# Performance work log

Hardware: AMD Instinct MI355X
Metric: run time of the kernel (lower is better)

Reference implementation:

```python
import jax, jax.numpy as jnp
import numpy as np

B, H, S, D = 2, 16, 2048, 64

def setup_inputs() -> dict:
    key = jax.random.key(0)
    kq, kk, kv = jax.random.split(key, 3)
    q = jax.random.normal(kq, (B, H, S, D), dtype=jnp.float32)
    k = jax.random.normal(kk, (B, H, S, D), dtype=jnp.float32)
    v = jax.random.normal(kv, (B, H, S, D), dtype=jnp.float32)
    return {"q": q, "k": k, "v": v}

def reference(q, k, v):
    scale = q.shape[-1] ** -0.5
    # sim: [b, h, i, j]
    sim = jnp.einsum('bhid,bhjd->bhij', q, k) * scale
    attn = jax.nn.softmax(sim, axis=-1)
    out = jnp.einsum('bhij,bhjd->bhid', attn, v)
    return out
```

## Files before the change

kernel.cpp:

```cpp
#include <hip/hip_runtime.h>

typedef _Float16 f16;
typedef f16 f16x4 __attribute__((ext_vector_type(4)));
typedef f16 f16x8 __attribute__((ext_vector_type(8)));
typedef float f32x4 __attribute__((ext_vector_type(4)));

static constexpr int S_LEN  = 2048;
static constexpr int D_DIM  = 64;
static constexpr int NTILE  = 64;
static constexpr int MBLOCK = 128;
static constexpr int NT     = S_LEN / NTILE;
static constexpr int FRAG_F16 = 512;
static constexpr int TILE_F16 = 8 * FRAG_F16;
static constexpr float SCALE_LOG2E = 0.1803368801111204f;
static constexpr float SHIFT = 4.0f;

#define MFMA32(a,b,c) __builtin_amdgcn_mfma_f32_16x16x32_f16((a),(b),(c),0,0,0)
#define MFMA16(a,b,c) __builtin_amdgcn_mfma_f32_16x16x16f16((a),(b),(c),0,0,0)

__device__ __forceinline__ void async_copy16(const f16* g, f16* l) {
  __builtin_amdgcn_global_load_lds(
      (const __attribute__((address_space(1))) unsigned int*)g,
      (__attribute__((address_space(3))) unsigned int*)l, 16, 0, 0);
}

__global__ __launch_bounds__(256)
void prepack(const float* __restrict__ kg, const float* __restrict__ vg,
             f16* __restrict__ kws, f16* __restrict__ vws) {
  const int h  = blockIdx.x >> 5;
  const int tl = blockIdx.x & 31;
  const int t = threadIdx.x, l = t & 63, gsel = t >> 6;
  const int L = l & 15, quad = l >> 4;
  const float* kh = kg + (size_t)h * S_LEN * D_DIM;
  const float* vh = vg + (size_t)h * S_LEN * D_DIM;
  f16* kout = kws + (size_t)(h * 32 + tl) * TILE_F16;
  f16* vout = vws + (size_t)(h * 32 + tl) * TILE_F16;
#pragma unroll
  for (int gg = 0; gg < 2; ++gg) {
    const int g = gsel + gg * 4;
    {
      const int jt = g >> 1, kc = g & 1;
      const float* src = kh + (size_t)(tl * 64 + jt * 16 + L) * D_DIM + kc * 32 + quad * 8;
      float4 a = *(const float4*)src;
      float4 b = *(const float4*)(src + 4);
      f16x8 o;
      o[0] = (f16)a.x; o[1] = (f16)a.y; o[2] = (f16)a.z; o[3] = (f16)a.w;
      o[4] = (f16)b.x; o[5] = (f16)b.y; o[6] = (f16)b.z; o[7] = (f16)b.w;
      *(f16x8*)&kout[(g * 64 + l) * 8] = o;
    }
    {
      const int jtp = g & 1, dt = g >> 1;
      const int d = dt * 16 + L;
      f16x8 o;
#pragma unroll
      for (int s = 0; s < 4; ++s) {
        const size_t j0 = (size_t)(tl * 64 + jtp * 32 + quad * 4 + s);
        o[s]     = (f16)vh[j0 * D_DIM + d];
        o[s + 4] = (f16)vh[(j0 + 16) * D_DIM + d];
      }
      *(f16x8*)&vout[(g * 64 + l) * 8] = o;
    }
  }
}

__global__ __launch_bounds__(256, 2)
void attn_fwd(const float* __restrict__ qg, const f16* __restrict__ kws,
              const f16* __restrict__ vws, float* __restrict__ og) {
  const int bh = blockIdx.x >> 4;
  const int qt = blockIdx.x & 15;
  const float* qh = qg + (size_t)bh * S_LEN * D_DIM;
  float*       oh = og + (size_t)bh * S_LEN * D_DIM;
  const f16* ktiles = kws + (size_t)bh * 32 * TILE_F16;
  const f16* vtiles = vws + (size_t)bh * 32 * TILE_F16;

  const int tid  = threadIdx.x;
  const int wave = tid >> 6;
  const int lane = tid & 63;
  const int L    = lane & 15;
  const int quad = lane >> 4;

  __shared__ __attribute__((aligned(16))) f16 Kbuf[2][TILE_F16];
  __shared__ __attribute__((aligned(16))) f16 Vbuf[2][TILE_F16];

  f16x8 qf[2][2];
  const int qrow0 = qt * MBLOCK + wave * 32;
#pragma unroll
  for (int qs = 0; qs < 2; ++qs)
#pragma unroll
    for (int kc = 0; kc < 2; ++kc) {
      const float* src = qh + (size_t)(qrow0 + qs * 16 + L) * D_DIM + kc * 32 + quad * 8;
      float4 x0 = *(const float4*)src;
      float4 x1 = *(const float4*)(src + 4);
      f16x8 t;
      t[0] = (f16)x0.x; t[1] = (f16)x0.y; t[2] = (f16)x0.z; t[3] = (f16)x0.w;
      t[4] = (f16)x1.x; t[5] = (f16)x1.y; t[6] = (f16)x1.z; t[7] = (f16)x1.w;
      qf[qs][kc] = t;
    }

  f32x4 oacc[2][4];
#pragma unroll
  for (int qs = 0; qs < 2; ++qs)
#pragma unroll
    for (int dt = 0; dt < 4; ++dt) oacc[qs][dt] = (f32x4){0.f, 0.f, 0.f, 0.f};
  float lsum[2] = {0.f, 0.f};

  {
    const f16* kp = ktiles;  const f16* vp = vtiles;
    async_copy16(kp + ((wave    ) * 64 + lane) * 8, &Kbuf[0][(wave    ) * FRAG_F16]);
    async_copy16(kp + ((wave + 4) * 64 + lane) * 8, &Kbuf[0][(wave + 4) * FRAG_F16]);
    async_copy16(vp + ((wave    ) * 64 + lane) * 8, &Vbuf[0][(wave    ) * FRAG_F16]);
    async_copy16(vp + ((wave + 4) * 64 + lane) * 8, &Vbuf[0][(wave + 4) * FRAG_F16]);
  }

  for (int kt = 0; kt < NT; ++kt) {
    const int cur = kt & 1;
    __syncthreads();

    if (kt + 1 < NT) {
      const int nxt = cur ^ 1;
      const f16* kp = ktiles + (size_t)(kt + 1) * TILE_F16;
      const f16* vp = vtiles + (size_t)(kt + 1) * TILE_F16;
      async_copy16(kp + ((wave    ) * 64 + lane) * 8, &Kbuf[nxt][(wave    ) * FRAG_F16]);
      async_copy16(kp + ((wave + 4) * 64 + lane) * 8, &Kbuf[nxt][(wave + 4) * FRAG_F16]);
      async_copy16(vp + ((wave    ) * 64 + lane) * 8, &Vbuf[nxt][(wave    ) * FRAG_F16]);
      async_copy16(vp + ((wave + 4) * 64 + lane) * 8, &Vbuf[nxt][(wave + 4) * FRAG_F16]);
    }

    f32x4 sfr[2][4];
#pragma unroll
    for (int qs = 0; qs < 2; ++qs)
#pragma unroll
      for (int jt = 0; jt < 4; ++jt) sfr[qs][jt] = (f32x4){0.f, 0.f, 0.f, 0.f};
#pragma unroll
    for (int jt = 0; jt < 4; ++jt)
#pragma unroll
      for (int kc = 0; kc < 2; ++kc) {
        f16x8 af = *(const f16x8*)&Kbuf[cur][(jt * 2 + kc) * FRAG_F16 + lane * 8];
        sfr[0][jt] = MFMA32(af, qf[0][kc], sfr[0][jt]);
        sfr[1][jt] = MFMA32(af, qf[1][kc], sfr[1][jt]);
      }

    f16x4 pf[2][4];
#pragma unroll
    for (int qs = 0; qs < 2; ++qs)
#pragma unroll
      for (int jt = 0; jt < 4; ++jt) {
        const float p0 = __builtin_amdgcn_exp2f(__builtin_fmaf(sfr[qs][jt][0], SCALE_LOG2E, -SHIFT));
        const float p1 = __builtin_amdgcn_exp2f(__builtin_fmaf(sfr[qs][jt][1], SCALE_LOG2E, -SHIFT));
        const float p2 = __builtin_amdgcn_exp2f(__builtin_fmaf(sfr[qs][jt][2], SCALE_LOG2E, -SHIFT));
        const float p3 = __builtin_amdgcn_exp2f(__builtin_fmaf(sfr[qs][jt][3], SCALE_LOG2E, -SHIFT));
        lsum[qs] += (p0 + p1) + (p2 + p3);
        pf[qs][jt] = (f16x4){(f16)p0, (f16)p1, (f16)p2, (f16)p3};
      }

#pragma unroll
    for (int dt = 0; dt < 4; ++dt)
#pragma unroll
      for (int jtp = 0; jtp < 2; ++jtp) {
        f16x8 vf = *(const f16x8*)&Vbuf[cur][(dt * 2 + jtp) * FRAG_F16 + lane * 8];
        f16x4 vlo = {vf[0], vf[1], vf[2], vf[3]};
        f16x4 vhi = {vf[4], vf[5], vf[6], vf[7]};
        oacc[0][dt] = MFMA16(pf[0][jtp * 2],     vlo, oacc[0][dt]);
        oacc[0][dt] = MFMA16(pf[0][jtp * 2 + 1], vhi, oacc[0][dt]);
        oacc[1][dt] = MFMA16(pf[1][jtp * 2],     vlo, oacc[1][dt]);
        oacc[1][dt] = MFMA16(pf[1][jtp * 2 + 1], vhi, oacc[1][dt]);
      }
  }

#pragma unroll
  for (int qs = 0; qs < 2; ++qs) {
    float l = lsum[qs];
    l += __shfl_xor(l, 16);
    l += __shfl_xor(l, 32);
#pragma unroll
    for (int r = 0; r < 4; ++r) {
      const float inv = 1.0f / __shfl(l, quad * 4 + r);
      float* dst = oh + (size_t)(qrow0 + qs * 16 + quad * 4 + r) * D_DIM + L;
#pragma unroll
      for (int dt = 0; dt < 4; ++dt)
        dst[dt * 16] = oacc[qs][dt][r] * inv;
    }
  }
}

extern "C" void kernel_launch(void* const* d_in, const int* in_sizes, int n_in,
                              void* d_out, int out_size, void* d_ws, size_t ws_size,
                              hipStream_t stream) {
  const float* q = (const float*)d_in[0];
  const float* k = (const float*)d_in[1];
  const float* v = (const float*)d_in[2];
  float* o = (float*)d_out;
  f16* kws = (f16*)d_ws;
  f16* vws = kws + (size_t)32 * 32 * TILE_F16;
  prepack<<<dim3(32 * 32), dim3(256), 0, stream>>>(k, v, kws, vws);
  attn_fwd<<<dim3(32 * 16), dim3(256), 0, stream>>>(q, kws, vws, o);
}
```

Before: 143.1 us.

## Split KV sequence across two wave groups per block and merge partial outputs

Doubles the block to 512 threads. Two groups of four waves each process half of the key/value tiles for the same 128 query rows, each with its own double-buffered LDS tiles. At the end, group 1 writes its unnormalized accumulators and row sums to shared memory, and group 0 combines them, normalizes and writes the output. The aim is more waves in flight per CU with only 512 blocks, for better latency hiding. The cost is an extra LDS reduction, wider __syncthreads barriers and a stricter occupancy hint.

```diff
diff --git a/kernel.cpp b/kernel.cpp
--- a/kernel.cpp
+++ b/kernel.cpp
@@ -10,6 +10,7 @@
 static constexpr int NTILE  = 64;
 static constexpr int MBLOCK = 128;
 static constexpr int NT     = S_LEN / NTILE;
+static constexpr int NT_STREAM = NT / 2;
 static constexpr int FRAG_F16 = 512;
 static constexpr int TILE_F16 = 8 * FRAG_F16;
 static constexpr float SCALE_LOG2E = 0.1803368801111204f;
@@ -63,7 +64,7 @@
   }
 }
 
-__global__ __launch_bounds__(256, 2)
+__global__ __launch_bounds__(512, 4)
 void attn_fwd(const float* __restrict__ qg, const f16* __restrict__ kws,
               const f16* __restrict__ vws, float* __restrict__ og) {
   const int bh = blockIdx.x >> 4;
@@ -73,17 +74,22 @@
   const f16* ktiles = kws + (size_t)bh * 32 * TILE_F16;
   const f16* vtiles = vws + (size_t)bh * 32 * TILE_F16;
 
-  const int tid  = threadIdx.x;
-  const int wave = tid >> 6;
-  const int lane = tid & 63;
-  const int L    = lane & 15;
-  const int quad = lane >> 4;
-
-  __shared__ __attribute__((aligned(16))) f16 Kbuf[2][TILE_F16];
-  __shared__ __attribute__((aligned(16))) f16 Vbuf[2][TILE_F16];
+  const int tid    = threadIdx.x;
+  const int wave   = tid >> 6;
+  const int stream = wave >> 2;
+  const int sw     = wave & 3;
+  const int lane   = tid & 63;
+  const int L      = lane & 15;
+  const int quad   = lane >> 4;
+
+  __shared__ __attribute__((aligned(16))) f16 smem[8 * TILE_F16];
+  f16* Kb[2] = {&smem[(stream * 2 + 0) * TILE_F16], &smem[(stream * 2 + 1) * TILE_F16]};
+  f16* Vb[2] = {&smem[(4 + stream * 2 + 0) * TILE_F16], &smem[(4 + stream * 2 + 1) * TILE_F16]};
+  const f16* kt_base = ktiles + (size_t)(stream * NT_STREAM) * TILE_F16;
+  const f16* vt_base = vtiles + (size_t)(stream * NT_STREAM) * TILE_F16;
 
   f16x8 qf[2][2];
-  const int qrow0 = qt * MBLOCK + wave * 32;
+  const int qrow0 = qt * MBLOCK + sw * 32;
 #pragma unroll
   for (int qs = 0; qs < 2; ++qs)
 #pragma unroll
@@ -104,26 +110,23 @@
     for (int dt = 0; dt < 4; ++dt) oacc[qs][dt] = (f32x4){0.f, 0.f, 0.f, 0.f};
   float lsum[2] = {0.f, 0.f};
 
-  {
-    const f16* kp = ktiles;  const f16* vp = vtiles;
-    async_copy16(kp + ((wave    ) * 64 + lane) * 8, &Kbuf[0][(wave    ) * FRAG_F16]);
-    async_copy16(kp + ((wave + 4) * 64 + lane) * 8, &Kbuf[0][(wave + 4) * FRAG_F16]);
-    async_copy16(vp + ((wave    ) * 64 + lane) * 8, &Vbuf[0][(wave    ) * FRAG_F16]);
-    async_copy16(vp + ((wave + 4) * 64 + lane) * 8, &Vbuf[0][(wave + 4) * FRAG_F16]);
-  }
-
-  for (int kt = 0; kt < NT; ++kt) {
+  async_copy16(kt_base + ((sw    ) * 64 + lane) * 8, Kb[0] + (sw    ) * FRAG_F16);
+  async_copy16(kt_base + ((sw + 4) * 64 + lane) * 8, Kb[0] + (sw + 4) * FRAG_F16);
+  async_copy16(vt_base + ((sw    ) * 64 + lane) * 8, Vb[0] + (sw    ) * FRAG_F16);
+  async_copy16(vt_base + ((sw + 4) * 64 + lane) * 8, Vb[0] + (sw + 4) * FRAG_F16);
+
+  for (int kt = 0; kt < NT_STREAM; ++kt) {
     const int cur = kt & 1;
     __syncthreads();
 
-    if (kt + 1 < NT) {
+    if (kt + 1 < NT_STREAM) {
       const int nxt = cur ^ 1;
-      const f16* kp = ktiles + (size_t)(kt + 1) * TILE_F16;
-      const f16* vp = vtiles + (size_t)(kt + 1) * TILE_F16;
-      async_copy16(kp + ((wave    ) * 64 + lane) * 8, &Kbuf[nxt][(wave    ) * FRAG_F16]);
-      async_copy16(kp + ((wave + 4) * 64 + lane) * 8, &Kbuf[nxt][(wave + 4) * FRAG_F16]);
-      async_copy16(vp + ((wave    ) * 64 + lane) * 8, &Vbuf[nxt][(wave    ) * FRAG_F16]);
-      async_copy16(vp + ((wave + 4) * 64 + lane) * 8, &Vbuf[nxt][(wave + 4) * FRAG_F16]);
+      const f16* kp = kt_base + (size_t)(kt + 1) * TILE_F16;
+      const f16* vp = vt_base + (size_t)(kt + 1) * TILE_F16;
+      async_copy16(kp + ((sw    ) * 64 + lane) * 8, Kb[nxt] + (sw    ) * FRAG_F16);
+      async_copy16(kp + ((sw + 4) * 64 + lane) * 8, Kb[nxt] + (sw + 4) * FRAG_F16);
+      async_copy16(vp + ((sw    ) * 64 + lane) * 8, Vb[nxt] + (sw    ) * FRAG_F16);
+      async_copy16(vp + ((sw + 4) * 64 + lane) * 8, Vb[nxt] + (sw + 4) * FRAG_F16);
     }
 
     f32x4 sfr[2][4];
@@ -135,7 +138,7 @@
     for (int jt = 0; jt < 4; ++jt)
 #pragma unroll
       for (int kc = 0; kc < 2; ++kc) {
-        f16x8 af = *(const f16x8*)&Kbuf[cur][(jt * 2 + kc) * FRAG_F16 + lane * 8];
+        f16x8 af = *(const f16x8*)&Kb[cur][(jt * 2 + kc) * FRAG_F16 + lane * 8];
         sfr[0][jt] = MFMA32(af, qf[0][kc], sfr[0][jt]);
         sfr[1][jt] = MFMA32(af, qf[1][kc], sfr[1][jt]);
       }
@@ -157,7 +160,7 @@
     for (int dt = 0; dt < 4; ++dt)
 #pragma unroll
       for (int jtp = 0; jtp < 2; ++jtp) {
-        f16x8 vf = *(const f16x8*)&Vbuf[cur][(dt * 2 + jtp) * FRAG_F16 + lane * 8];
+        f16x8 vf = *(const f16x8*)&Vb[cur][(dt * 2 + jtp) * FRAG_F16 + lane * 8];
         f16x4 vlo = {vf[0], vf[1], vf[2], vf[3]};
         f16x4 vhi = {vf[4], vf[5], vf[6], vf[7]};
         oacc[0][dt] = MFMA16(pf[0][jtp * 2],     vlo, oacc[0][dt]);
@@ -167,18 +170,44 @@
       }
   }
 
+  float lq[2];
 #pragma unroll
   for (int qs = 0; qs < 2; ++qs) {
     float l = lsum[qs];
     l += __shfl_xor(l, 16);
     l += __shfl_xor(l, 32);
-#pragma unroll
-    for (int r = 0; r < 4; ++r) {
-      const float inv = 1.0f / __shfl(l, quad * 4 + r);
-      float* dst = oh + (size_t)(qrow0 + qs * 16 + quad * 4 + r) * D_DIM + L;
+    lq[qs] = l;
+  }
+
+  __syncthreads();
+  float* Osc = (float*)smem;
+  float* lsc = Osc + 4 * 32 * 65;
+  if (stream == 1) {
+#pragma unroll
+    for (int qs = 0; qs < 2; ++qs) {
 #pragma unroll
       for (int dt = 0; dt < 4; ++dt)
-        dst[dt * 16] = oacc[qs][dt][r] * inv;
+#pragma unroll
+        for (int r = 0; r < 4; ++r)
+          Osc[(sw * 32 + qs * 16 + quad * 4 + r) * 65 + dt * 16 + L] = oacc[qs][dt][r];
+      if (quad == 0) lsc[sw * 32 + qs * 16 + L] = lq[qs];
+    }
+  }
+  __syncthreads();
+  if (stream == 0) {
+#pragma unroll
+    for (int qs = 0; qs < 2; ++qs) {
+      const float ltot = lq[qs] + lsc[sw * 32 + qs * 16 + L];
+#pragma unroll
+      for (int r = 0; r < 4; ++r) {
+        const float inv = 1.0f / __shfl(ltot, quad * 4 + r);
+        float* dst = oh + (size_t)(qrow0 + qs * 16 + quad * 4 + r) * D_DIM + L;
+#pragma unroll
+        for (int dt = 0; dt < 4; ++dt) {
+          const float up = Osc[(sw * 32 + qs * 16 + quad * 4 + r) * 65 + dt * 16 + L];
+          dst[dt * 16] = (oacc[qs][dt][r] + up) * inv;
+        }
+      }
     }
   }
 }
@@ -193,5 +222,5 @@
   f16* kws = (f16*)d_ws;
   f16* vws = kws + (size_t)32 * 32 * TILE_F16;
   prepack<<<dim3(32 * 32), dim3(256), 0, stream>>>(k, v, kws, vws);
-  attn_fwd<<<dim3(32 * 16), dim3(256), 0, stream>>>(q, kws, vws, o);
-}
+  attn_fwd<<<dim3(32 * 16), dim3(512), 0, stream>>>(q, kws, vws, o);
+}
```

Result: no change. 143.8 us (+0.5%).
